# Kernel tuning notes

Hardware: AMD Instinct MI355X
Metric: run time of the kernel (lower is better)

The kernel has to match this reference:

```python
import jax, jax.numpy as jnp
import numpy as np

SEQ_LEN = 720
PRED_LEN = 720
CHANNEL_DIM = 321
BATCH = 64


def setup_inputs() -> dict:
    key = jax.random.key(0)
    kx, kw, kb = jax.random.split(key, 3)
    x = jax.random.normal(kx, (BATCH, SEQ_LEN, CHANNEL_DIM), dtype=jnp.float32)
    # per-channel Linear(seq_len, pred_len): weight [C, pred_len, seq_len], bias [C, pred_len]
    bound = 1.0 / np.sqrt(SEQ_LEN)
    W = jax.random.uniform(kw, (CHANNEL_DIM, PRED_LEN, SEQ_LEN), minval=-bound, maxval=bound, dtype=jnp.float32)
    b = jax.random.uniform(kb, (CHANNEL_DIM, PRED_LEN), minval=-bound, maxval=bound, dtype=jnp.float32)
    return {"x": x, "W": W, "b": b}


def reference(x, W, b):
    # x: [B, S, C]; per-channel linear along the time axis.
    # torch: x.transpose(1,2) -> [B, C, S]; y[:, i] = Linear_i(x[:, i]); transpose back.
    # Batched grouped GEMM over channels in one einsum.
    y = jnp.einsum('bsc,cps->bcp', x, W) + b  # [B, C, P]
    return y.transpose(0, 2, 1)  # [B, P, C]
```

## Files before the change

### kernel.cpp

```cpp
#include <hip/hip_runtime.h>
#include <hip/hip_bf16.h>


#define SEQ   720
#define PRED  720
#define CH    321
#define BATCH 64
#define RTOT  (BATCH*SEQ)
#define BN    144
#define NTILE 5
#define NCHUNK 21
#define NGROUP (NCHUNK*NTILE)

typedef __attribute__((ext_vector_type(8))) short short8;
typedef __attribute__((ext_vector_type(4))) float f32x4;
typedef __attribute__((ext_vector_type(4))) unsigned short us4;
typedef unsigned int u32;

__device__ __forceinline__ short bf16bits(float f) {
    return __builtin_bit_cast(short, __float2bfloat16(f));
}

__device__ __forceinline__ void gload16(const void* g, void* l) {
    __builtin_amdgcn_global_load_lds((const __attribute__((address_space(1))) u32*)g,
                                     (__attribute__((address_space(3))) u32*)l, 16, 0, 0);
}

__global__ __launch_bounds__(256) void xpose_kernel(const float* __restrict__ x,
                                                    unsigned short* __restrict__ xt) {
    __shared__ float tile[64][33];
    const int bid = blockIdx.x;
    const int rt = bid % (RTOT/64);
    const int ct = bid / (RTOT/64);
    const int r0 = rt*64, c0 = ct*32;
    const int t  = threadIdx.x;
    const int cl = t & 31, rl0 = t >> 5;
    const int cg = c0 + cl;
    if (cg < CH) {
#pragma unroll
        for (int j = 0; j < 8; ++j) {
            int rl = rl0 + j*8;
            tile[rl][cl] = x[(size_t)(r0+rl)*CH + cg];
        }
    }
    __syncthreads();
#pragma unroll
    for (int j = 0; j < 8; ++j) {
        int idx = t + j*256;
        int c_l = idx >> 6;
        int r_l = idx & 63;
        if (c0 + c_l < CH)
            xt[(size_t)(c0+c_l)*RTOT + r0 + r_l] = (unsigned short)bf16bits(tile[r_l][c_l]);
    }
}

template<bool STAGED>
__global__ __launch_bounds__(192) void gemm_lds_kernel(
        const float* __restrict__ W, const float* __restrict__ bias,
        const unsigned short* __restrict__ xt, void* __restrict__ outp) {
    __shared__ __align__(16) float          Bl[2][BN*32];
    __shared__ __align__(16) unsigned short Al[2][64*32];

    const int bid  = blockIdx.x;
    const int xcd  = bid & 7;
    const int rest = bid >> 3;
    const int gi   = rest >> 4;
    const int coff = rest & 15;
    const int g    = xcd + 8*gi;
    if (g >= NGROUP) return;
    const int chunk = g % NCHUNK;
    const int pt    = g / NCHUNK;
    const int c     = chunk*16 + coff;
    if (c >= CH) return;
    const int p0 = pt * BN;

    const int tid  = threadIdx.x;
    const int wv   = tid >> 6;
    const int lane = tid & 63;
    const int row  = lane & 15;
    const int kch  = lane >> 4;
    const int nb   = p0 + wv*48;

    const float* Wc          = W  + (size_t)c * ((size_t)PRED * SEQ);
    const unsigned short* Xc = xt + (size_t)c * RTOT;

    auto stage = [&](int buf, int kk) {
#pragma unroll
        for (int i = 0; i < 6; ++i) {
            const int slot = i*192 + tid;
            const int r    = slot >> 3;
            int sc = (slot & 7) ^ (r & 7);
            if (kk == 22) sc &= 3;
            gload16(Wc + (size_t)(p0 + r)*SEQ + kk*32 + sc*4,
                    &Bl[buf][(i*192 + (tid & ~63)) * 4]);
        }
#pragma unroll
        for (int i = 0; i < 2; ++i) {
            const int slot = (i*192 + tid) & 255;
            const int r    = slot >> 2;
            int sc = (slot & 3) ^ (r & 3);
            if (kk == 22) sc &= 1;
            gload16(Xc + (size_t)r*SEQ + kk*32 + sc*8,
                    &Al[buf][((i*192 + (tid & ~63)) & 255) * 8]);
        }
    };

    f32x4 acc[4][3] = {};

    auto compute = [&](int buf, bool tail) {
        short8 Af[4];
#pragma unroll
        for (int mi = 0; mi < 4; ++mi) {
            const int r2 = mi*16 + row;
            const int qa = kch ^ (r2 & 3);
            Af[mi] = *reinterpret_cast<const short8*>(&Al[buf][r2*32 + qa*8]);
        }
        short8 Bf[3];
#pragma unroll
        for (int ni = 0; ni < 3; ++ni) {
            const int r2  = wv*48 + ni*16 + row;
            const int qlo = (2*kch)     ^ (r2 & 7);
            const int qhi = (2*kch + 1) ^ (r2 & 7);
            f32x4 lo = *reinterpret_cast<const f32x4*>(&Bl[buf][r2*32 + qlo*4]);
            f32x4 hi = *reinterpret_cast<const f32x4*>(&Bl[buf][r2*32 + qhi*4]);
            short8 v;
#pragma unroll
            for (int j = 0; j < 4; ++j) { v[j] = bf16bits(lo[j]); v[4+j] = bf16bits(hi[j]); }
            Bf[ni] = v;
        }
        if (tail && kch >= 2) {
            short8 z = {};
            Bf[0] = z; Bf[1] = z; Bf[2] = z;
        }
#pragma unroll
        for (int mi = 0; mi < 4; ++mi)
#pragma unroll
            for (int ni = 0; ni < 3; ++ni)
                acc[mi][ni] = __builtin_amdgcn_mfma_f32_16x16x32_bf16(
                                  Af[mi], Bf[ni], acc[mi][ni], 0, 0, 0);
    };

    stage(0, 0);
    stage(1, 1);
    for (int k = 0; k < 22; ++k) {
        const int buf = k & 1;
        asm volatile("s_waitcnt vmcnt(8)" ::: "memory");
        __builtin_amdgcn_sched_barrier(0);
        __builtin_amdgcn_s_barrier();

        short8 dummy;
        compute(buf, false);
        asm volatile("s_waitcnt lgkmcnt(0)" ::: "memory");
        __builtin_amdgcn_sched_barrier(0);
        __builtin_amdgcn_s_barrier();
        if (k <= 20) stage(buf, k + 2);
    }
    {
        asm volatile("s_waitcnt vmcnt(0)" ::: "memory");
        __builtin_amdgcn_sched_barrier(0);
        __builtin_amdgcn_s_barrier();
        compute(0, true);
    }

    const int col   = lane & 15;
    const int rquad = lane >> 4;
    if (STAGED) {
        unsigned short* stg = (unsigned short*)outp;
#pragma unroll
        for (int ni = 0; ni < 3; ++ni) {
            const int p = nb + ni*16 + col;
            const float bv = bias[(size_t)c*PRED + p];
#pragma unroll
            for (int mi = 0; mi < 4; ++mi) {
                us4 u;
#pragma unroll
                for (int r = 0; r < 4; ++r)
                    u[r] = (unsigned short)bf16bits(acc[mi][ni][r] + bv);
                *reinterpret_cast<us4*>(
                    stg + ((size_t)c*PRED + p)*BATCH + mi*16 + rquad*4) = u;
            }
        }
    } else {
        float* outf = (float*)outp;
#pragma unroll
        for (int ni = 0; ni < 3; ++ni) {
            const int p = nb + ni*16 + col;
            const float bv = bias[(size_t)c*PRED + p];
#pragma unroll
            for (int mi = 0; mi < 4; ++mi)
#pragma unroll
                for (int r = 0; r < 4; ++r) {
                    const int b = mi*16 + rquad*4 + r;
                    outf[((size_t)b*PRED + p)*CH + c] = acc[mi][ni][r] + bv;
                }
        }
    }
}

__global__ __launch_bounds__(192) void gemm_fallback_kernel(
        const float* __restrict__ W, const float* __restrict__ bias,
        const float* __restrict__ x, float* __restrict__ outp) {
    const int bid  = blockIdx.x;
    const int g    = (bid & 7) + 8*((bid >> 3) >> 4);
    const int coff = (bid >> 3) & 15;
    if (g >= NGROUP) return;
    const int c  = (g % NCHUNK)*16 + coff;
    if (c >= CH) return;
    const int p0 = (g / NCHUNK) * BN;
    const int tid = threadIdx.x, wv = tid >> 6, lane = tid & 63;
    const int row = lane & 15, kch = lane >> 4, nb = p0 + wv*48;
    const float* Wc = W + (size_t)c * ((size_t)PRED * SEQ);
    f32x4 acc[4][3] = {};
    for (int k = 0; k < 23; ++k) {
        const int kc = (k == 22) ? (kch & 1) : kch;
        const int s  = k*32 + kc*8;
        short8 Af[4], Bf[3];
#pragma unroll
        for (int mi = 0; mi < 4; ++mi) {
            short8 v;
#pragma unroll
            for (int j = 0; j < 8; ++j)
                v[j] = bf16bits(x[((size_t)(mi*16 + row)*SEQ + s + j)*CH + c]);
            Af[mi] = v;
        }
#pragma unroll
        for (int ni = 0; ni < 3; ++ni) {
            const float* p = Wc + (size_t)(nb + ni*16 + row)*SEQ + s;
            short8 v;
#pragma unroll
            for (int j = 0; j < 4; ++j) { v[j] = bf16bits(p[j]); v[4+j] = bf16bits(p[4+j]); }
            Bf[ni] = v;
        }
        if (k == 22 && kch >= 2) { short8 z = {}; Bf[0] = z; Bf[1] = z; Bf[2] = z; }
#pragma unroll
        for (int mi = 0; mi < 4; ++mi)
#pragma unroll
            for (int ni = 0; ni < 3; ++ni)
                acc[mi][ni] = __builtin_amdgcn_mfma_f32_16x16x32_bf16(
                                  Af[mi], Bf[ni], acc[mi][ni], 0, 0, 0);
    }
    const int col = lane & 15, rquad = lane >> 4;
#pragma unroll
    for (int ni = 0; ni < 3; ++ni) {
        const int p = nb + ni*16 + col;
        const float bv = bias[(size_t)c*PRED + p];
#pragma unroll
        for (int mi = 0; mi < 4; ++mi)
#pragma unroll
            for (int r = 0; r < 4; ++r)
                outp[((size_t)(mi*16 + rquad*4 + r)*PRED + p)*CH + c] = acc[mi][ni][r] + bv;
    }
}

__global__ __launch_bounds__(256) void unstage_kernel(const unsigned short* __restrict__ stage,
                                                      float* __restrict__ out) {
    const int p  = blockIdx.x;
    const int c0 = blockIdx.y * 128;
    const int cn = (CH - c0 < 128) ? (CH - c0) : 128;
    __shared__ float tl[128][65];
    const int t = threadIdx.x;
    {
        const int b   = t & 63;
        const int ci0 = t >> 6;
        for (int ci = ci0; ci < cn; ci += 4) {
            unsigned short us = stage[((size_t)(c0+ci)*PRED + p)*BATCH + b];
            tl[ci][b] = __builtin_bit_cast(float, (u32)us << 16);
        }
    }
    __syncthreads();
    {
        const int cl = t & 127;
        const int b0 = t >> 7;
        if (cl < cn)
#pragma unroll
            for (int bb = b0; bb < BATCH; bb += 2)
                out[((size_t)bb*PRED + p)*CH + c0 + cl] = tl[cl][bb];
    }
}

extern "C" void kernel_launch(void* const* d_in, const int* in_sizes, int n_in,
                              void* d_out, int out_size, void* d_ws, size_t ws_size,
                              hipStream_t stream) {
    const float* x    = (const float*)d_in[0];
    const float* W    = (const float*)d_in[1];
    const float* bias = (const float*)d_in[2];
    float* out        = (float*)d_out;

    const size_t xt_bytes    = (size_t)CH * RTOT * sizeof(unsigned short);
    const size_t stage_bytes = (size_t)CH * PRED * BATCH * sizeof(unsigned short);
    const int gemm_blocks = 8 * 14 * 16;

    if (ws_size >= xt_bytes + stage_bytes) {
        unsigned short* xtp = (unsigned short*)d_ws;
        unsigned short* stg = (unsigned short*)((char*)d_ws + xt_bytes);
        xpose_kernel<<<dim3((RTOT/64) * 11), dim3(256), 0, stream>>>(x, xtp);
        gemm_lds_kernel<true><<<dim3(gemm_blocks), dim3(192), 0, stream>>>(
            W, bias, xtp, stg);
        unstage_kernel<<<dim3(PRED, 3), dim3(256), 0, stream>>>(stg, out);
    } else if (ws_size >= xt_bytes) {
        unsigned short* xtp = (unsigned short*)d_ws;
        xpose_kernel<<<dim3((RTOT/64) * 11), dim3(256), 0, stream>>>(x, xtp);
        gemm_lds_kernel<false><<<dim3(gemm_blocks), dim3(192), 0, stream>>>(
            W, bias, xtp, out);
    } else {
        gemm_fallback_kernel<<<dim3(gemm_blocks), dim3(192), 0, stream>>>(
            W, bias, x, out);
    }
}
```

Before: 225.2 us.

## Replace 3-wave GEMM blocks with single-wave blocks and deeper K tiles

The grouped GEMM now runs one 64-thread wavefront per block. Each block covers a 48-wide pred tile for one channel and uses 64-wide K stages instead of 32, so the K loop runs 11 iterations plus a tail. Workgroup barriers and the XCD-aware block mapping are dropped, and the block count grows to CH*15. This cuts synchronisation and raises the number of independent blocks. In exchange, the X tile staged in LDS is no longer shared across three waves, so X is loaded more times overall, and each wave must issue more loads per stage.

```diff
diff --git a/kernel.cpp b/kernel.cpp
--- a/kernel.cpp
+++ b/kernel.cpp
@@ -7,10 +7,11 @@
 #define CH    321
 #define BATCH 64
 #define RTOT  (BATCH*SEQ)
+#define BN1   48
+#define NT1   15
 #define BN    144
-#define NTILE 5
 #define NCHUNK 21
-#define NGROUP (NCHUNK*NTILE)
+#define NGROUP (NCHUNK*5)
 
 typedef __attribute__((ext_vector_type(8))) short short8;
 typedef __attribute__((ext_vector_type(4))) float f32x4;
@@ -55,80 +56,64 @@
 }
 
 template<bool STAGED>
-__global__ __launch_bounds__(192) void gemm_lds_kernel(
+__global__ __launch_bounds__(64) void gemm1w_kernel(
         const float* __restrict__ W, const float* __restrict__ bias,
         const unsigned short* __restrict__ xt, void* __restrict__ outp) {
-    __shared__ __align__(16) float          Bl[2][BN*32];
-    __shared__ __align__(16) unsigned short Al[2][64*32];
-
-    const int bid  = blockIdx.x;
-    const int xcd  = bid & 7;
-    const int rest = bid >> 3;
-    const int gi   = rest >> 4;
-    const int coff = rest & 15;
-    const int g    = xcd + 8*gi;
-    if (g >= NGROUP) return;
-    const int chunk = g % NCHUNK;
-    const int pt    = g / NCHUNK;
-    const int c     = chunk*16 + coff;
-    if (c >= CH) return;
-    const int p0 = pt * BN;
-
-    const int tid  = threadIdx.x;
-    const int wv   = tid >> 6;
-    const int lane = tid & 63;
-    const int row  = lane & 15;
-    const int kch  = lane >> 4;
-    const int nb   = p0 + wv*48;
+    __shared__ __align__(16) float          Bl[2][BN1*64];
+    __shared__ __align__(16) unsigned short Al[2][64*64];
+
+    const int bid = blockIdx.x;
+    const int c   = bid / NT1;
+    const int pt  = bid % NT1;
+    const int p0  = pt * BN1;
+    const int lane = threadIdx.x & 63;
+    const int row = lane & 15, kch = lane >> 4;
 
     const float* Wc          = W  + (size_t)c * ((size_t)PRED * SEQ);
     const unsigned short* Xc = xt + (size_t)c * RTOT;
 
     auto stage = [&](int buf, int kk) {
-#pragma unroll
-        for (int i = 0; i < 6; ++i) {
-            const int slot = i*192 + tid;
-            const int r    = slot >> 3;
-            int sc = (slot & 7) ^ (r & 7);
-            if (kk == 22) sc &= 3;
-            gload16(Wc + (size_t)(p0 + r)*SEQ + kk*32 + sc*4,
-                    &Bl[buf][(i*192 + (tid & ~63)) * 4]);
-        }
-#pragma unroll
-        for (int i = 0; i < 2; ++i) {
-            const int slot = (i*192 + tid) & 255;
-            const int r    = slot >> 2;
-            int sc = (slot & 3) ^ (r & 3);
-            if (kk == 22) sc &= 1;
-            gload16(Xc + (size_t)r*SEQ + kk*32 + sc*8,
-                    &Al[buf][((i*192 + (tid & ~63)) & 255) * 8]);
+        const bool tail = (kk == 11);
+#pragma unroll
+        for (int i = 0; i < 12; ++i) {
+            const int r = 4*i + (lane >> 4);
+            int sc = (lane & 15) ^ (r & 15);
+            if (tail) sc &= 3;
+            gload16(Wc + (size_t)(p0 + r)*SEQ + kk*64 + sc*4, &Bl[buf][i*256]);
+        }
+#pragma unroll
+        for (int i = 0; i < 8; ++i) {
+            const int r = 8*i + (lane >> 3);
+            int sc = (lane & 7) ^ (r & 7);
+            if (tail) sc &= 1;
+            gload16(Xc + (size_t)r*SEQ + kk*64 + sc*8, &Al[buf][i*512]);
         }
     };
 
     f32x4 acc[4][3] = {};
 
-    auto compute = [&](int buf, bool tail) {
+    auto compute = [&](int buf, int s, bool ztail) {
         short8 Af[4];
 #pragma unroll
         for (int mi = 0; mi < 4; ++mi) {
             const int r2 = mi*16 + row;
-            const int qa = kch ^ (r2 & 3);
-            Af[mi] = *reinterpret_cast<const short8*>(&Al[buf][r2*32 + qa*8]);
+            const int qa = (s*4 + kch) ^ (r2 & 7);
+            Af[mi] = *reinterpret_cast<const short8*>(&Al[buf][r2*64 + qa*8]);
         }
         short8 Bf[3];
 #pragma unroll
         for (int ni = 0; ni < 3; ++ni) {
-            const int r2  = wv*48 + ni*16 + row;
-            const int qlo = (2*kch)     ^ (r2 & 7);
-            const int qhi = (2*kch + 1) ^ (r2 & 7);
-            f32x4 lo = *reinterpret_cast<const f32x4*>(&Bl[buf][r2*32 + qlo*4]);
-            f32x4 hi = *reinterpret_cast<const f32x4*>(&Bl[buf][r2*32 + qhi*4]);
+            const int r2  = ni*16 + row;
+            const int qlo = (s*8 + 2*kch)     ^ (r2 & 15);
+            const int qhi = (s*8 + 2*kch + 1) ^ (r2 & 15);
+            f32x4 lo = *reinterpret_cast<const f32x4*>(&Bl[buf][r2*64 + qlo*4]);
+            f32x4 hi = *reinterpret_cast<const f32x4*>(&Bl[buf][r2*64 + qhi*4]);
             short8 v;
 #pragma unroll
             for (int j = 0; j < 4; ++j) { v[j] = bf16bits(lo[j]); v[4+j] = bf16bits(hi[j]); }
             Bf[ni] = v;
         }
-        if (tail && kch >= 2) {
+        if (ztail && kch >= 2) {
             short8 z = {};
             Bf[0] = z; Bf[1] = z; Bf[2] = z;
         }
@@ -142,24 +127,20 @@
 
     stage(0, 0);
     stage(1, 1);
-    for (int k = 0; k < 22; ++k) {
+    for (int k = 0; k < 11; ++k) {
         const int buf = k & 1;
-        asm volatile("s_waitcnt vmcnt(8)" ::: "memory");
+        asm volatile("s_waitcnt vmcnt(20)" ::: "memory");
         __builtin_amdgcn_sched_barrier(0);
-        __builtin_amdgcn_s_barrier();
-
-        short8 dummy;
-        compute(buf, false);
+        compute(buf, 0, false);
+        compute(buf, 1, false);
         asm volatile("s_waitcnt lgkmcnt(0)" ::: "memory");
         __builtin_amdgcn_sched_barrier(0);
-        __builtin_amdgcn_s_barrier();
-        if (k <= 20) stage(buf, k + 2);
+        if (k <= 9) stage(buf, k + 2);
     }
     {
         asm volatile("s_waitcnt vmcnt(0)" ::: "memory");
         __builtin_amdgcn_sched_barrier(0);
-        __builtin_amdgcn_s_barrier();
-        compute(0, true);
+        compute(1, 0, true);
     }
 
     const int col   = lane & 15;
@@ -168,7 +149,7 @@
         unsigned short* stg = (unsigned short*)outp;
 #pragma unroll
         for (int ni = 0; ni < 3; ++ni) {
-            const int p = nb + ni*16 + col;
+            const int p = p0 + ni*16 + col;
             const float bv = bias[(size_t)c*PRED + p];
 #pragma unroll
             for (int mi = 0; mi < 4; ++mi) {
@@ -184,7 +165,7 @@
         float* outf = (float*)outp;
 #pragma unroll
         for (int ni = 0; ni < 3; ++ni) {
-            const int p = nb + ni*16 + col;
+            const int p = p0 + ni*16 + col;
             const float bv = bias[(size_t)c*PRED + p];
 #pragma unroll
             for (int mi = 0; mi < 4; ++mi)
@@ -288,22 +269,19 @@
 
     const size_t xt_bytes    = (size_t)CH * RTOT * sizeof(unsigned short);
     const size_t stage_bytes = (size_t)CH * PRED * BATCH * sizeof(unsigned short);
-    const int gemm_blocks = 8 * 14 * 16;
 
     if (ws_size >= xt_bytes + stage_bytes) {
         unsigned short* xtp = (unsigned short*)d_ws;
         unsigned short* stg = (unsigned short*)((char*)d_ws + xt_bytes);
         xpose_kernel<<<dim3((RTOT/64) * 11), dim3(256), 0, stream>>>(x, xtp);
-        gemm_lds_kernel<true><<<dim3(gemm_blocks), dim3(192), 0, stream>>>(
-            W, bias, xtp, stg);
+        gemm1w_kernel<true><<<dim3(CH * NT1), dim3(64), 0, stream>>>(W, bias, xtp, stg);
         unstage_kernel<<<dim3(PRED, 3), dim3(256), 0, stream>>>(stg, out);
     } else if (ws_size >= xt_bytes) {
         unsigned short* xtp = (unsigned short*)d_ws;
         xpose_kernel<<<dim3((RTOT/64) * 11), dim3(256), 0, stream>>>(x, xtp);
-        gemm_lds_kernel<false><<<dim3(gemm_blocks), dim3(192), 0, stream>>>(
-            W, bias, xtp, out);
+        gemm1w_kernel<false><<<dim3(CH * NT1), dim3(64), 0, stream>>>(W, bias, xtp, out);
     } else {
-        gemm_fallback_kernel<<<dim3(gemm_blocks), dim3(192), 0, stream>>>(
+        gemm_fallback_kernel<<<dim3(8 * 14 * 16), dim3(192), 0, stream>>>(
             W, bias, x, out);
     }
 }
```

After: 217.7 us. 3.3% less time.
